# Optimization experiments

Measured on AMD Instinct MI355X. Metric: run time of the kernel, lower is better.

## Reference

```python
import jax, jax.numpy as jnp
import numpy as np

TEMPERATURE = 0.07
EPS = 1e-8  # torch CosineSimilarity eps


def setup_inputs() -> dict:
    key = jax.random.key(0)
    features = jax.random.normal(key, (16, 1024, 512), dtype=jnp.float32)
    return {"features": features}


def reference(features):
    """Vectorized equivalent of the original double Python loop.

    For each b and each t in [1, T-2]:
      anchor = f[b,t], positive = f[b,t+1]
      negatives = all frames j with j < t-1 or j >= t+2  (excludes t-1, t, t+1)
      loss_bt = -log( exp(cos(a,p)/T) / (exp(cos(a,p)/T) + sum_j exp(cos(a,n_j)/T)) )
    Returns mean over all (b, t) pairs (neg pool is non-empty for all t when T > 3).
    """
    B, T, D = features.shape
    norm = jnp.maximum(jnp.linalg.norm(features, axis=-1, keepdims=True), EPS)
    n = features / norm  # [B, T, D]
    # full pairwise cosine-sim logits, scaled by temperature
    sim = jnp.einsum('btd,bsd->bts', n, n) / TEMPERATURE  # [B, T, T]

    t_idx = jnp.arange(1, T - 1)            # anchors t = 1 .. T-2
    j_idx = jnp.arange(T)
    # negatives: j in [0, t-1) union [t+2, T)  -> excludes t-1, t, t+1
    neg_mask = (j_idx[None, :] < t_idx[:, None] - 1) | (j_idx[None, :] >= t_idx[:, None] + 2)  # [T-2, T]

    logits = sim[:, 1:T - 1, :]                                   # [B, T-2, T]
    pos = logits[:, jnp.arange(T - 2), jnp.arange(2, T)]          # sim[b, t, t+1] -> [B, T-2]
    neg_logits = jnp.where(neg_mask[None], logits, -jnp.inf)
    lse_neg = jax.nn.logsumexp(neg_logits, axis=-1)               # log sum_j exp(neg_sim)
    # -log(exp(pos)/(exp(pos)+negsum)) = logaddexp(pos, lse_neg) - pos
    loss_bt = jnp.logaddexp(pos, lse_neg) - pos                   # [B, T-2]
    return jnp.mean(loss_bt)
```

## Files before the change

### kernel.cpp

```cpp
#include <hip/hip_runtime.h>
#include <hip/hip_bf16.h>

#define B_ 16
#define T_ 1024
#define D_ 512
#define EPS_ 1e-8f
#define SCALE2 20.609929155566063f
#define LN2_ 0.6931471805599453f

#define BT 64
#define NB 16
#define NPAIR (NB * (NB + 1) / 2)
#define NKIT 16

typedef __attribute__((ext_vector_type(8))) short short8;
typedef __attribute__((ext_vector_type(4))) float floatx4;

typedef __attribute__((address_space(1))) const unsigned int g_u32;
typedef __attribute__((address_space(3))) unsigned int l_u32;

__device__ __forceinline__ void glds16(const void* g, void* l) {
    __builtin_amdgcn_global_load_lds((g_u32*)g, (l_u32*)l, 16, 0, 0);
}

__device__ __forceinline__ unsigned short f2bf(float x) {
    unsigned u = __float_as_uint(x);
    return (unsigned short)((u + 0x7fffu + ((u >> 16) & 1u)) >> 16);
}

__global__ __launch_bounds__(256) void norm_kernel(const float* __restrict__ f,
                                                   unsigned short* __restrict__ nrm,
                                                   float* __restrict__ rs_g,
                                                   float* __restrict__ rp_g,
                                                   float* __restrict__ out) {
    const int gi = blockIdx.x * 256 + threadIdx.x;
    if (gi < B_ * T_) { rs_g[gi] = 0.0f; rp_g[gi] = 0.0f; }
    if (gi == 0) out[0] = 0.0f;

    const int row  = blockIdx.x * 4 + (threadIdx.x >> 6);
    const int lane = threadIdx.x & 63;
    const size_t off = (size_t)row * D_ + lane * 8;
    const float4 v0 = *(const float4*)(f + off);
    const float4 v1 = *(const float4*)(f + off + 4);
    float ss = v0.x*v0.x + v0.y*v0.y + v0.z*v0.z + v0.w*v0.w
             + v1.x*v1.x + v1.y*v1.y + v1.z*v1.z + v1.w*v1.w;
    #pragma unroll
    for (int o = 32; o >= 1; o >>= 1) ss += __shfl_xor(ss, o, 64);
    const float sc = 1.0f / fmaxf(sqrtf(ss), EPS_);
    ushort4 w0, w1;
    w0.x = f2bf(v0.x*sc); w0.y = f2bf(v0.y*sc); w0.z = f2bf(v0.z*sc); w0.w = f2bf(v0.w*sc);
    w1.x = f2bf(v1.x*sc); w1.y = f2bf(v1.y*sc); w1.z = f2bf(v1.z*sc); w1.w = f2bf(v1.w*sc);
    *(ushort4*)(nrm + off)     = w0;
    *(ushort4*)(nrm + off + 4) = w1;
}

__global__ __launch_bounds__(64) void loss_kernel(const unsigned short* __restrict__ nrm,
                                                  float* __restrict__ rs_g,
                                                  float* __restrict__ rp_g) {
    const int slot = blockIdx.x & 15;
    int u = blockIdx.x >> 4;
    const int b = ((slot & 7) << 1) | (slot >> 3);
    int bi = 0, rem = NB;
    while (u >= rem) { u -= rem; --rem; ++bi; }
    const int bj   = bi + u;
    const bool diag = (bi == bj);
    const bool near = (bj - bi) <= 1;

    const int t0 = bi * BT;
    const int j0 = bj * BT;
    const char* base = (const char*)(nrm + (size_t)b * T_ * D_);

    __shared__ __align__(16) unsigned short Al[2][2048];
    __shared__ __align__(16) unsigned short Bl[2][2048];

    const int l = threadIdx.x & 63;

    const int r   = l >> 2;
    const int gsw = (l & 3) ^ ((r >> 1) & 3);
    const char* sA[4];
    const char* sB[4];
    #pragma unroll
    for (int i = 0; i < 4; ++i) {
        sA[i] = base + (size_t)(t0 + i * 16 + r) * 1024 + gsw * 16;
        sB[i] = base + (size_t)(j0 + i * 16 + r) * 1024 + gsw * 16;
    }

#define ISSUE(P) do {                                                  \
    _Pragma("unroll")                                                  \
    for (int i_ = 0; i_ < 4; ++i_) {                                   \
        glds16(sA[i_], (char*)Al[P] + i_ * 1024);                      \
        sA[i_] += 64;                                                  \
    }                                                                  \
    if (!diag) {                                                       \
        _Pragma("unroll")                                              \
        for (int i_ = 0; i_ < 4; ++i_) {                               \
            glds16(sB[i_], (char*)Bl[P] + i_ * 1024);                  \
            sB[i_] += 64;                                              \
        }                                                              \
    }                                                                  \
} while (0)

    const int m  = l & 15;
    const int kq = l >> 4;
    const int rdoff = m * 64 + ((kq ^ ((m >> 1) & 3)) << 4);

    floatx4 acc[4][4] = {};

    ISSUE(0);

    #pragma unroll 2
    for (int kit = 0; kit < NKIT; ++kit) {
        __syncthreads();
        if (kit + 1 < NKIT) ISSUE((kit + 1) & 1);

        const char* pa = (const char*)Al[kit & 1] + rdoff;
        const char* pb = (diag ? (const char*)Al[kit & 1]
                               : (const char*)Bl[kit & 1]) + rdoff;
        short8 af[4], bf[4];
        #pragma unroll
        for (int mi = 0; mi < 4; ++mi) af[mi] = *(const short8*)(pa + mi * 1024);
        #pragma unroll
        for (int ni = 0; ni < 4; ++ni) bf[ni] = *(const short8*)(pb + ni * 1024);

        #pragma unroll
        for (int mi = 0; mi < 4; ++mi)
            #pragma unroll
            for (int ni = 0; ni < 4; ++ni)
                acc[mi][ni] = __builtin_amdgcn_mfma_f32_16x16x32_bf16(
                    af[mi], bf[ni], acc[mi][ni], 0, 0, 0);
    }
#undef ISSUE

    const int lrow = l >> 4;
    const int lcol = l & 15;
    const int bT   = b * T_;
    float cs[4] = {0.f, 0.f, 0.f, 0.f};

    #pragma unroll
    for (int mi = 0; mi < 4; ++mi) {
        #pragma unroll
        for (int rg = 0; rg < 4; ++rg) {
            const int t = t0 + mi * 16 + lrow * 4 + rg;
            float rsum = 0.f;
            #pragma unroll
            for (int ni = 0; ni < 4; ++ni) {
                const int j  = j0 + ni * 16 + lcol;
                const float s2 = acc[mi][ni][rg] * SCALE2;
                const float e  = exp2f(s2);
                if (j < t - 1 || j > t + 1) { rsum += e; cs[ni] += e; }
                if (near && j == t + 1) atomicAdd(&rp_g[bT + t], s2);
            }
            #pragma unroll
            for (int o = 8; o >= 1; o >>= 1) rsum += __shfl_xor(rsum, o, 64);
            if (lcol == 0) atomicAdd(&rs_g[bT + t], rsum);
        }
    }
    if (!diag) {
        #pragma unroll
        for (int ni = 0; ni < 4; ++ni) {
            float c = cs[ni];
            c += __shfl_xor(c, 16, 64);
            c += __shfl_xor(c, 32, 64);
            if (lrow == 0)
                atomicAdd(&rs_g[bT + j0 + ni * 16 + lcol], c);
        }
    }
}

__global__ __launch_bounds__(256) void fin_kernel(const float* __restrict__ rs_g,
                                                  const float* __restrict__ rp_g,
                                                  float* __restrict__ out) {
    const int idx = blockIdx.x * 256 + threadIdx.x;
    float v = 0.0f;
    if (idx < B_ * T_) {
        const int t = idx & (T_ - 1);
        if (t >= 1 && t <= T_ - 2) {
            const float p2 = rp_g[idx];
            const float s  = rs_g[idx];
            v = (log2f(exp2f(p2) + s) - p2) * LN2_;
        }
    }
    #pragma unroll
    for (int o = 32; o >= 1; o >>= 1) v += __shfl_xor(v, o, 64);
    __shared__ float ws_[4];
    if ((threadIdx.x & 63) == 0) ws_[threadIdx.x >> 6] = v;
    __syncthreads();
    if (threadIdx.x == 0) {
        const float scale = 1.0f / (float)(B_ * (T_ - 2));
        atomicAdd(out, (ws_[0] + ws_[1] + ws_[2] + ws_[3]) * scale);
    }
}

extern "C" void kernel_launch(void* const* d_in, const int* in_sizes, int n_in,
                              void* d_out, int out_size, void* d_ws, size_t ws_size,
                              hipStream_t stream) {
    const float* feat = (const float*)d_in[0];
    float* out = (float*)d_out;

    unsigned short* nrm = (unsigned short*)d_ws;
    float* rs_g = (float*)((char*)d_ws + (size_t)B_ * T_ * D_ * sizeof(unsigned short));
    float* rp_g = rs_g + B_ * T_;

    norm_kernel<<<B_ * T_ / 4, 256, 0, stream>>>(feat, nrm, rs_g, rp_g, out);
    loss_kernel<<<NPAIR * B_, 64, 0, stream>>>(nrm, rs_g, rp_g);
    fin_kernel<<<(B_ * T_ + 255) / 256, 256, 0, stream>>>(rs_g, rp_g, out);
}
```

Before: 101.8 us.

## Quantize normalized features to FP8 e4m3 and use scaled 16x16x128 MFMA

Normalized features are stored as FP8 e4m3, pre-scaled by 16, instead of bf16. The Gram matrix is computed with the scaled f8f6f4 MFMA (K=128), with block scales that undo the prescale, and LDS is restaged into a 4-slot ring. This halves the intermediate memory traffic and cuts MFMA issue count, at the cost of lower precision in the cosine similarities, which is amplified by the 1/0.07 temperature before exponentiation.

```diff
diff --git a/kernel.cpp b/kernel.cpp
--- a/kernel.cpp
+++ b/kernel.cpp
@@ -1,5 +1,6 @@
 #include <hip/hip_runtime.h>
 #include <hip/hip_bf16.h>
+#include <hip/hip_fp8.h>
 
 #define B_ 16
 #define T_ 1024
@@ -11,9 +12,11 @@
 #define BT 64
 #define NB 16
 #define NPAIR (NB * (NB + 1) / 2)
-#define NKIT 16
-
-typedef __attribute__((ext_vector_type(8))) short short8;
+#define NKIT 4
+#define SCL 0x7B7B7B7B
+
+typedef __attribute__((ext_vector_type(4))) int   int4v;
+typedef __attribute__((ext_vector_type(8))) int   int8v;
 typedef __attribute__((ext_vector_type(4))) float floatx4;
 
 typedef __attribute__((address_space(1))) const unsigned int g_u32;
@@ -23,13 +26,13 @@
     __builtin_amdgcn_global_load_lds((g_u32*)g, (l_u32*)l, 16, 0, 0);
 }
 
-__device__ __forceinline__ unsigned short f2bf(float x) {
-    unsigned u = __float_as_uint(x);
-    return (unsigned short)((u + 0x7fffu + ((u >> 16) & 1u)) >> 16);
+__device__ __forceinline__ unsigned char f2e4m3(float x) {
+    __hip_fp8_e4m3 q(x);
+    return (unsigned char)q.__x;
 }
 
 __global__ __launch_bounds__(256) void norm_kernel(const float* __restrict__ f,
-                                                   unsigned short* __restrict__ nrm,
+                                                   unsigned char* __restrict__ nrm,
                                                    float* __restrict__ rs_g,
                                                    float* __restrict__ rp_g,
                                                    float* __restrict__ out) {
@@ -46,15 +49,20 @@
              + v1.x*v1.x + v1.y*v1.y + v1.z*v1.z + v1.w*v1.w;
     #pragma unroll
     for (int o = 32; o >= 1; o >>= 1) ss += __shfl_xor(ss, o, 64);
-    const float sc = 1.0f / fmaxf(sqrtf(ss), EPS_);
-    ushort4 w0, w1;
-    w0.x = f2bf(v0.x*sc); w0.y = f2bf(v0.y*sc); w0.z = f2bf(v0.z*sc); w0.w = f2bf(v0.w*sc);
-    w1.x = f2bf(v1.x*sc); w1.y = f2bf(v1.y*sc); w1.z = f2bf(v1.z*sc); w1.w = f2bf(v1.w*sc);
-    *(ushort4*)(nrm + off)     = w0;
-    *(ushort4*)(nrm + off + 4) = w1;
-}
-
-__global__ __launch_bounds__(64) void loss_kernel(const unsigned short* __restrict__ nrm,
+    const float sc = 16.0f / fmaxf(sqrtf(ss), EPS_);
+    unsigned int w0 =  (unsigned int)f2e4m3(v0.x*sc)
+                    | ((unsigned int)f2e4m3(v0.y*sc) << 8)
+                    | ((unsigned int)f2e4m3(v0.z*sc) << 16)
+                    | ((unsigned int)f2e4m3(v0.w*sc) << 24);
+    unsigned int w1 =  (unsigned int)f2e4m3(v1.x*sc)
+                    | ((unsigned int)f2e4m3(v1.y*sc) << 8)
+                    | ((unsigned int)f2e4m3(v1.z*sc) << 16)
+                    | ((unsigned int)f2e4m3(v1.w*sc) << 24);
+    uint2 w; w.x = w0; w.y = w1;
+    *(uint2*)(nrm + (size_t)row * D_ + lane * 8) = w;
+}
+
+__global__ __launch_bounds__(64) void loss_kernel(const unsigned char* __restrict__ nrm,
                                                   float* __restrict__ rs_g,
                                                   float* __restrict__ rp_g) {
     const int slot = blockIdx.x & 15;
@@ -70,10 +78,11 @@
     const int j0 = bj * BT;
     const char* base = (const char*)(nrm + (size_t)b * T_ * D_);
 
-    __shared__ __align__(16) unsigned short Al[2][2048];
-    __shared__ __align__(16) unsigned short Bl[2][2048];
+    __shared__ __align__(16) char Ar[4][4096];
+    __shared__ __align__(16) char Br[4][4096];
 
     const int l = threadIdx.x & 63;
+    const int m = l & 15;
 
     const int r   = l >> 2;
     const int gsw = (l & 3) ^ ((r >> 1) & 3);
@@ -81,53 +90,60 @@
     const char* sB[4];
     #pragma unroll
     for (int i = 0; i < 4; ++i) {
-        sA[i] = base + (size_t)(t0 + i * 16 + r) * 1024 + gsw * 16;
-        sB[i] = base + (size_t)(j0 + i * 16 + r) * 1024 + gsw * 16;
-    }
-
-#define ISSUE(P) do {                                                  \
+        sA[i] = base + (size_t)(t0 + i * 16 + r) * 512 + gsw * 16;
+        sB[i] = base + (size_t)(j0 + i * 16 + r) * 512 + gsw * 16;
+    }
+
+#define ISSUE(S) do {                                                  \
     _Pragma("unroll")                                                  \
-    for (int i_ = 0; i_ < 4; ++i_) {                                   \
-        glds16(sA[i_], (char*)Al[P] + i_ * 1024);                      \
-        sA[i_] += 64;                                                  \
-    }                                                                  \
+    for (int i_ = 0; i_ < 4; ++i_)                                     \
+        glds16(sA[i_] + (S) * 64, Ar[(S) & 3] + i_ * 1024);            \
     if (!diag) {                                                       \
         _Pragma("unroll")                                              \
-        for (int i_ = 0; i_ < 4; ++i_) {                               \
-            glds16(sB[i_], (char*)Bl[P] + i_ * 1024);                  \
-            sB[i_] += 64;                                              \
-        }                                                              \
+        for (int i_ = 0; i_ < 4; ++i_)                                 \
+            glds16(sB[i_] + (S) * 64, Br[(S) & 3] + i_ * 1024);        \
     }                                                                  \
 } while (0)
 
-    const int m  = l & 15;
-    const int kq = l >> 4;
-    const int rdoff = m * 64 + ((kq ^ ((m >> 1) & 3)) << 4);
+    const int kqh  = l >> 5;
+    const int ph0  = (2 * ((l >> 4) & 1)) ^ ((m >> 1) & 3);
+    const int rd0  = m * 64 + ph0 * 16;
+    const int rd1  = m * 64 + (ph0 ^ 1) * 16;
 
     floatx4 acc[4][4] = {};
 
-    ISSUE(0);
-
-    #pragma unroll 2
-    for (int kit = 0; kit < NKIT; ++kit) {
+    ISSUE(0); ISSUE(1);
+
+    #pragma unroll
+    for (int j = 0; j < NKIT; ++j) {
         __syncthreads();
-        if (kit + 1 < NKIT) ISSUE((kit + 1) & 1);
-
-        const char* pa = (const char*)Al[kit & 1] + rdoff;
-        const char* pb = (diag ? (const char*)Al[kit & 1]
-                               : (const char*)Bl[kit & 1]) + rdoff;
-        short8 af[4], bf[4];
-        #pragma unroll
-        for (int mi = 0; mi < 4; ++mi) af[mi] = *(const short8*)(pa + mi * 1024);
-        #pragma unroll
-        for (int ni = 0; ni < 4; ++ni) bf[ni] = *(const short8*)(pb + ni * 1024);
+        if (j < NKIT - 1) { ISSUE(2 * j + 2); ISSUE(2 * j + 3); }
+
+        const char* As = Ar[(2 * j + kqh) & 3];
+        const char* Bs = diag ? Ar[(2 * j + kqh) & 3] : Br[(2 * j + kqh) & 3];
+        int8v af[4], bf[4];
+        #pragma unroll
+        for (int mi = 0; mi < 4; ++mi) {
+            int4v lo = *(const int4v*)(As + mi * 1024 + rd0);
+            int4v hi = *(const int4v*)(As + mi * 1024 + rd1);
+            af[mi] = __builtin_shufflevector(lo, hi, 0, 1, 2, 3, 4, 5, 6, 7);
+        }
+        #pragma unroll
+        for (int ni = 0; ni < 4; ++ni) {
+            int4v lo = *(const int4v*)(Bs + ni * 1024 + rd0);
+            int4v hi = *(const int4v*)(Bs + ni * 1024 + rd1);
+            bf[ni] = __builtin_shufflevector(lo, hi, 0, 1, 2, 3, 4, 5, 6, 7);
+        }
 
         #pragma unroll
         for (int mi = 0; mi < 4; ++mi)
             #pragma unroll
             for (int ni = 0; ni < 4; ++ni)
-                acc[mi][ni] = __builtin_amdgcn_mfma_f32_16x16x32_bf16(
-                    af[mi], bf[ni], acc[mi][ni], 0, 0, 0);
+                acc[mi][ni] = __builtin_amdgcn_mfma_scale_f32_16x16x128_f8f6f4(
+                    af[mi], bf[ni], acc[mi][ni],
+                    0, 0,
+                    0, SCL,
+                    0, SCL);
     }
 #undef ISSUE
 
@@ -197,8 +213,8 @@
     const float* feat = (const float*)d_in[0];
     float* out = (float*)d_out;
 
-    unsigned short* nrm = (unsigned short*)d_ws;
-    float* rs_g = (float*)((char*)d_ws + (size_t)B_ * T_ * D_ * sizeof(unsigned short));
+    unsigned char* nrm = (unsigned char*)d_ws;
+    float* rs_g = (float*)((char*)d_ws + (size_t)B_ * T_ * D_);
     float* rp_g = rs_g + B_ * T_;
 
     norm_kernel<<<B_ * T_ / 4, 256, 0, stream>>>(feat, nrm, rs_g, rp_g, out);
```

After: 101.0 us. About the same (-0.8%).
